# Performance work log

Measured on AMD Instinct MI355X. Metric: run time of the kernel, lower is better.

## Reference

```python
import jax, jax.numpy as jnp
import numpy as np

B, F, H, E, C, K = 32768, 1024, 512, 10, 10, 4  # batch, in_features, hidden, f_enc, num_classes, n_branches


def setup_inputs() -> dict:
    key = jax.random.key(0)
    ks = jax.random.split(key, 12)
    def rn(k, shape, scale):
        return jax.random.normal(k, shape, jnp.float32) * scale
    return {
        "w0": rn(ks[0], (B, F), 1.0),
        "w1": rn(ks[1], (B, F), 1.0),
        "w2": rn(ks[2], (B, F), 1.0),
        "w3": rn(ks[3], (B, F), 1.0),
        # 4 branch linears in -> hidden, stacked on leading axis
        "Wlin": rn(ks[4], (K, H, F), F ** -0.5),
        "blin": jnp.zeros((K, H), jnp.float32),
        # per-branch Q/K/V projections hidden -> f_enc
        "Wq": rn(ks[5], (K, E, H), H ** -0.5),
        "bq": jnp.zeros((K, E), jnp.float32),
        "Wk": rn(ks[6], (K, E, H), H ** -0.5),
        "bk": jnp.zeros((K, E), jnp.float32),
        "Wv": rn(ks[7], (K, E, H), H ** -0.5),
        "bv": jnp.zeros((K, E), jnp.float32),
        # 4 final classifier heads f_enc -> num_classes
        "Wfin": rn(ks[8], (K, C, E), E ** -0.5),
        "bfin": jnp.zeros((K, C), jnp.float32),
    }


def reference(w0, w1, w2, w3, Wlin, blin, Wq, bq, Wk, bk, Wv, bv, Wfin, bfin):
    # dropout is identity in eval mode
    w = jnp.stack([w0, w1, w2, w3], axis=1)              # [B,K,F]
    h = jnp.einsum('bkf,khf->bkh', w, Wlin) + blin        # [B,K,H]
    q = jnp.einsum('bkh,keh->bke', h, Wq) + bq            # [B,K,E]
    k_enc = jnp.einsum('bkh,keh->bke', h, Wk) + bk        # [B,K,E]
    v = jnp.einsum('bkh,keh->bke', h, Wv) + bv            # [B,K,E]
    # einsum 'bij,bil->bjl' contracts the branch axis (i == K)
    attn = jnp.einsum('bke,bkl->bel', q, k_enc) / np.float32(np.sqrt(E))  # [B,E,E]
    attn = jax.nn.softmax(attn, axis=1)                   # torch Softmax(dim=1)
    att_out = jnp.einsum('bnm,bkm->bkn', attn, v)         # [B,K,E]
    w0o = att_out[:, 0, :]                                # original uses index 0 for all four heads
    logits = jnp.einsum('be,kce->bkc', w0o, Wfin) + bfin  # [B,K,C]
    outputs = jnp.mean(jax.nn.softmax(logits, axis=-1), axis=1)  # 0.25 * sum of 4 softmaxed heads
    return (outputs, attn)
```

## Files before the change

kernel.cpp:

```cpp
#include <hip/hip_runtime.h>
#include <stdint.h>

#define B_ROWS 32768
#define F_DIM  1024
#define H_DIM  512
#define RS     32832

typedef __attribute__((ext_vector_type(4))) float    floatx4;
typedef __attribute__((ext_vector_type(2))) __fp16   fp16x2;
typedef __attribute__((ext_vector_type(8))) _Float16 halfx8;

__device__ __forceinline__ void async_load16(const void* g, void* l) {
    __builtin_amdgcn_global_load_lds(
        (const __attribute__((address_space(1))) void*)g,
        (__attribute__((address_space(3))) void*)l, 16, 0, 0);
}

__global__ __launch_bounds__(64) void k_prep(
    const float* __restrict__ Wlin, const float* __restrict__ blin,
    const float* __restrict__ Wq, const float* __restrict__ Wk,
    const float* __restrict__ Wv, const float* __restrict__ bq,
    const float* __restrict__ bk, const float* __restrict__ bv,
    ushort* __restrict__ Wcomb16, float* __restrict__ bcomb)
{
    __shared__ float sw_[H_DIM];
    __shared__ float sbl[H_DIM];
    const int bx = blockIdx.x;
    const int k  = bx >> 7;
    const int d  = (bx >> 2) & 31;
    const int qd = bx & 3;
    const int t  = threadIdx.x;
    const int col = qd * 256 + t * 4;
    ushort4* outp = (ushort4*)(Wcomb16 + (((size_t)(k * 32 + d)) << 10) + col);

    if (d >= 30) {
        ushort4 z; z.x = z.y = z.z = z.w = 0;
        *outp = z;
        if (qd == 0 && t == 0) bcomb[k * 32 + d] = 0.f;
        return;
    }

    const float* wrow; float bias;
    if (d < 10)      { wrow = Wq + (size_t)(k * 10 + d) * H_DIM;      bias = bq[k * 10 + d]; }
    else if (d < 20) { wrow = Wk + (size_t)(k * 10 + d - 10) * H_DIM; bias = bk[k * 10 + d - 10]; }
    else             { wrow = Wv + (size_t)(k * 10 + d - 20) * H_DIM; bias = bv[k * 10 + d - 20]; }

    const float* bl = blin + (size_t)k * H_DIM;
    for (int i = t; i < H_DIM; i += 64) { sw_[i] = wrow[i]; sbl[i] = bl[i]; }
    __syncthreads();

    const float* wl = Wlin + (((size_t)k * H_DIM) << 10) + col;

    floatx4 acc0 = {0.f,0.f,0.f,0.f}, acc1 = {0.f,0.f,0.f,0.f};
    float ba0 = 0.f, ba1 = 0.f;
    #pragma unroll 8
    for (int h = 0; h < H_DIM; h += 2) {
        const float s0 = sw_[h], s1 = sw_[h + 1];
        const floatx4 x0 = *(const floatx4*)(wl + ((size_t)h << 10));
        const floatx4 x1 = *(const floatx4*)(wl + ((size_t)(h + 1) << 10));
        acc0 += x0 * s0;
        acc1 += x1 * s1;
        ba0 += s0 * sbl[h];
        ba1 += s1 * sbl[h + 1];
    }
    const floatx4 acc = acc0 + acc1;
    union { _Float16 h[4]; ushort4 u; } o;
    o.h[0] = (_Float16)acc.x; o.h[1] = (_Float16)acc.y;
    o.h[2] = (_Float16)acc.z; o.h[3] = (_Float16)acc.w;
    *outp = o.u;
    if (qd == 0 && t == 0) bcomb[k * 32 + d] = bias + ba0 + ba1;
}

__global__ __launch_bounds__(512, 4) void k_main(
    const float* __restrict__ w0, const float* __restrict__ w1,
    const float* __restrict__ w2, const float* __restrict__ w3,
    const ushort* __restrict__ Wcomb16, const float* __restrict__ bcomb,
    float* __restrict__ qkv_t)
{
    __shared__ ushort Bs[32 * 1024];

    const int tid     = threadIdx.x;
    const int bx      = blockIdx.x;
    const int k       = bx & 3;
    const int rowBase = (bx >> 2) * 256;

    const float* A = (k == 0) ? w0 : (k == 1) ? w1 : (k == 2) ? w2 : w3;

    #pragma unroll
    for (int it = 0; it < 8; ++it) {
        const int s   = it * 512 + tid;
        const int row = s >> 7;
        const int g   = (s & 127) ^ (row & 7);
        async_load16(Wcomb16 + (((size_t)(k * 32 + row)) << 10) + g * 8,
                     (ushort*)Bs + (size_t)s * 8);
    }
    __syncthreads();

    const int wv = tid >> 6;
    const int ln = tid & 63;
    const int lr = ln & 15;
    const int lq = ln >> 4;
    const int sw = lr & 7;

    const float* aP0 = A + (size_t)(rowBase + wv * 32 + lr) * F_DIM + lq * 8;
    const float* aP1 = aP0 + (size_t)16 * F_DIM;

    floatx4 acc[2][2] = {};

#define LOADC(kc, b0, b1, b2, b3) do {                       \
    b0 = *(const floatx4*)(aP0 + (kc));                      \
    b1 = *(const floatx4*)(aP0 + (kc) + 4);                  \
    b2 = *(const floatx4*)(aP1 + (kc));                      \
    b3 = *(const floatx4*)(aP1 + (kc) + 4);                  \
} while (0)

#define COMPUTE(t, b0, b1, b2, b3) do {                                      \
    union { fp16x2 h2[4]; halfx8 h8; } u0, u1;                               \
    u0.h2[0] = __builtin_amdgcn_cvt_pkrtz(b0.x, b0.y);                       \
    u0.h2[1] = __builtin_amdgcn_cvt_pkrtz(b0.z, b0.w);                       \
    u0.h2[2] = __builtin_amdgcn_cvt_pkrtz(b1.x, b1.y);                       \
    u0.h2[3] = __builtin_amdgcn_cvt_pkrtz(b1.z, b1.w);                       \
    u1.h2[0] = __builtin_amdgcn_cvt_pkrtz(b2.x, b2.y);                       \
    u1.h2[1] = __builtin_amdgcn_cvt_pkrtz(b2.z, b2.w);                       \
    u1.h2[2] = __builtin_amdgcn_cvt_pkrtz(b3.x, b3.y);                       \
    u1.h2[3] = __builtin_amdgcn_cvt_pkrtz(b3.z, b3.w);                       \
    const int slot_ = (((t) * 4 + lq) ^ sw) * 8;                             \
    const halfx8 bf0 = *(const halfx8*)&Bs[(lr << 10) + slot_];              \
    const halfx8 bf1 = *(const halfx8*)&Bs[((16 + lr) << 10) + slot_];       \
    acc[0][0] = __builtin_amdgcn_mfma_f32_16x16x32_f16(u0.h8, bf0, acc[0][0], 0, 0, 0); \
    acc[0][1] = __builtin_amdgcn_mfma_f32_16x16x32_f16(u0.h8, bf1, acc[0][1], 0, 0, 0); \
    acc[1][0] = __builtin_amdgcn_mfma_f32_16x16x32_f16(u1.h8, bf0, acc[1][0], 0, 0, 0); \
    acc[1][1] = __builtin_amdgcn_mfma_f32_16x16x32_f16(u1.h8, bf1, acc[1][1], 0, 0, 0); \
} while (0)

    floatx4 a0, a1, a2, a3, c0, c1, c2, c3;
    LOADC(0, a0, a1, a2, a3);
    #pragma unroll 2
    for (int t = 0; t < 32; t += 2) {
        LOADC((t + 1) * 32, c0, c1, c2, c3);
        COMPUTE(t, a0, a1, a2, a3);
        if (t + 2 < 32) LOADC((t + 2) * 32, a0, a1, a2, a3);
        COMPUTE(t + 1, c0, c1, c2, c3);
    }
#undef LOADC
#undef COMPUTE

    const float* bc   = bcomb + k * 32;
    const int    dmax = (k == 0) ? 30 : 20;
    #pragma unroll
    for (int j = 0; j < 2; ++j) {
        const int d = j * 16 + lr;
        if (d < dmax) {
            const float bias = bc[d];
            float* outd = qkv_t + (size_t)(k * 30 + d) * RS;
            #pragma unroll
            for (int i = 0; i < 2; ++i) {
                const int r0 = rowBase + wv * 32 + i * 16 + lq * 4;
                floatx4 o = acc[i][j];
                o.x += bias; o.y += bias; o.z += bias; o.w += bias;
                *(floatx4*)(outd + r0) = o;
            }
        }
    }
}

__global__ __launch_bounds__(128) void k_final(
    const float* __restrict__ qkv_t, const float* __restrict__ Wfin,
    const float* __restrict__ bfin,
    float* __restrict__ outputs, float* __restrict__ attn)
{
    __shared__ float sW[400];
    __shared__ float sb[40];
    __shared__ float sA[128 * 101];
    const int t = threadIdx.x;
    for (int i = t; i < 400; i += 128) sW[i] = Wfin[i];
    if (t < 40) sb[t] = bfin[t];
    __syncthreads();

    const int b = blockIdx.x * 128 + t;
    const float* pt = qkv_t + b;
    float q[4][10], kk[4][10], v0[10];
    #pragma unroll
    for (int k = 0; k < 4; ++k)
        #pragma unroll
        for (int e = 0; e < 10; ++e) {
            q[k][e]  = pt[(size_t)(k * 30 + e) * RS];
            kk[k][e] = pt[(size_t)(k * 30 + 10 + e) * RS];
        }
    #pragma unroll
    for (int m = 0; m < 10; ++m) v0[m] = pt[(size_t)(20 + m) * RS];

    float out0[10];
    #pragma unroll
    for (int e = 0; e < 10; ++e) out0[e] = 0.f;
    float* sAr = &sA[t * 101];
    const float inv = 0.31622776601683794f;

    #pragma unroll
    for (int m = 0; m < 10; ++m) {
        float col[10]; float mx = -1e30f;
        #pragma unroll
        for (int e = 0; e < 10; ++e) {
            col[e] = (q[0][e]*kk[0][m] + q[1][e]*kk[1][m]
                    + q[2][e]*kk[2][m] + q[3][e]*kk[3][m]) * inv;
            mx = fmaxf(mx, col[e]);
        }
        float s = 0.f;
        #pragma unroll
        for (int e = 0; e < 10; ++e) { col[e] = __expf(col[e] - mx); s += col[e]; }
        const float r = 1.f / s;
        #pragma unroll
        for (int e = 0; e < 10; ++e) {
            const float a = col[e] * r;
            sAr[e * 10 + m] = a;
            out0[e] += a * v0[m];
        }
    }

    float oc[10];
    #pragma unroll
    for (int c = 0; c < 10; ++c) oc[c] = 0.f;
    #pragma unroll
    for (int k = 0; k < 4; ++k) {
        float lg[10]; float mx = -1e30f;
        #pragma unroll
        for (int c = 0; c < 10; ++c) {
            float s = sb[k * 10 + c];
            #pragma unroll
            for (int e = 0; e < 10; ++e) s += out0[e] * sW[(k * 10 + c) * 10 + e];
            lg[c] = s; mx = fmaxf(mx, s);
        }
        float s = 0.f;
        #pragma unroll
        for (int c = 0; c < 10; ++c) { lg[c] = __expf(lg[c] - mx); s += lg[c]; }
        const float r = 0.25f / s;
        #pragma unroll
        for (int c = 0; c < 10; ++c) oc[c] += lg[c] * r;
    }

    __syncthreads();
    const size_t abase = (size_t)blockIdx.x * 12800;
    for (int i = t; i < 12800; i += 128) {
        const int bl = i / 100;
        attn[abase + i] = sA[bl * 101 + (i - bl * 100)];
    }

    __syncthreads();
    #pragma unroll
    for (int c = 0; c < 10; ++c) sA[t * 11 + c] = oc[c];
    __syncthreads();
    const size_t obase = (size_t)blockIdx.x * 1280;
    for (int i = t; i < 1280; i += 128) {
        const int bl = i / 10;
        outputs[obase + i] = sA[bl * 11 + (i - bl * 10)];
    }
}

extern "C" void kernel_launch(void* const* d_in, const int* in_sizes, int n_in,
                              void* d_out, int out_size, void* d_ws, size_t ws_size,
                              hipStream_t stream) {
    const float* w0   = (const float*)d_in[0];
    const float* w1   = (const float*)d_in[1];
    const float* w2   = (const float*)d_in[2];
    const float* w3   = (const float*)d_in[3];
    const float* Wlin = (const float*)d_in[4];
    const float* blin = (const float*)d_in[5];
    const float* Wq   = (const float*)d_in[6];
    const float* bq   = (const float*)d_in[7];
    const float* Wk   = (const float*)d_in[8];
    const float* bk   = (const float*)d_in[9];
    const float* Wv   = (const float*)d_in[10];
    const float* bv   = (const float*)d_in[11];
    const float* Wfin = (const float*)d_in[12];
    const float* bfin = (const float*)d_in[13];

    char* ws = (char*)d_ws;
    ushort* Wcomb16 = (ushort*)ws;
    float*  bcomb   = (float*)(ws + ((size_t)256 << 10));
    float*  qkv_t   = (float*)(ws + ((size_t)1 << 20));

    float* outputs = (float*)d_out;
    float* attn    = outputs + (size_t)B_ROWS * 10;

    k_prep <<<512, 64,  0, stream>>>(Wlin, blin, Wq, Wk, Wv, bq, bk, bv, Wcomb16, bcomb);
    k_main <<<512, 512, 0, stream>>>(w0, w1, w2, w3, Wcomb16, bcomb, qkv_t);
    k_final<<<256, 128, 0, stream>>>(qkv_t, Wfin, bfin, outputs, attn);
}
```

Measured before the change: 583.1 us.

## Fuse projection GEMM with attention epilogue, keeping QKV in shared memory

Merges the main fp16 MFMA projection kernel and the attention/classifier kernel into one kernel. Each 512-thread block handles 128 rows and loops over the four branches, keeping the QKV activations in LDS instead of writing and rereading a transposed global buffer. The prep kernel also moves to 128-thread blocks covering half a row each. The grid shrinks to 256 blocks with about 130KB of LDS each, which lowers occupancy and latency hiding on the memory-bound input stream. Only a quarter of the threads do the attention epilogue, so that phase serialises after the GEMM.

After: 566.9 us. 1.03x faster.

```diff
diff --git a/kernel.cpp b/kernel.cpp
--- a/kernel.cpp
+++ b/kernel.cpp
@@ -4,7 +4,6 @@
 #define B_ROWS 32768
 #define F_DIM  1024
 #define H_DIM  512
-#define RS     32832
 
 typedef __attribute__((ext_vector_type(4))) float    floatx4;
 typedef __attribute__((ext_vector_type(2))) __fp16   fp16x2;
@@ -16,7 +15,7 @@
         (__attribute__((address_space(3))) void*)l, 16, 0, 0);
 }
 
-__global__ __launch_bounds__(64) void k_prep(
+__global__ __launch_bounds__(128) void k_prep(
     const float* __restrict__ Wlin, const float* __restrict__ blin,
     const float* __restrict__ Wq, const float* __restrict__ Wk,
     const float* __restrict__ Wv, const float* __restrict__ bq,
@@ -25,18 +24,18 @@
 {
     __shared__ float sw_[H_DIM];
     __shared__ float sbl[H_DIM];
-    const int bx = blockIdx.x;
-    const int k  = bx >> 7;
-    const int d  = (bx >> 2) & 31;
-    const int qd = bx & 3;
-    const int t  = threadIdx.x;
-    const int col = qd * 256 + t * 4;
+    const int bx   = blockIdx.x;
+    const int k    = bx >> 6;
+    const int d    = (bx >> 1) & 31;
+    const int half = bx & 1;
+    const int t    = threadIdx.x;
+    const int col  = half * 512 + t * 4;
     ushort4* outp = (ushort4*)(Wcomb16 + (((size_t)(k * 32 + d)) << 10) + col);
 
     if (d >= 30) {
         ushort4 z; z.x = z.y = z.z = z.w = 0;
         *outp = z;
-        if (qd == 0 && t == 0) bcomb[k * 32 + d] = 0.f;
+        if (half == 0 && t == 0) bcomb[k * 32 + d] = 0.f;
         return;
     }
 
@@ -46,7 +45,7 @@
     else             { wrow = Wv + (size_t)(k * 10 + d - 20) * H_DIM; bias = bv[k * 10 + d - 20]; }
 
     const float* bl = blin + (size_t)k * H_DIM;
-    for (int i = t; i < H_DIM; i += 64) { sw_[i] = wrow[i]; sbl[i] = bl[i]; }
+    for (int i = t; i < H_DIM; i += 128) { sw_[i] = wrow[i]; sbl[i] = bl[i]; }
     __syncthreads();
 
     const float* wl = Wlin + (((size_t)k * H_DIM) << 10) + col;
@@ -68,33 +67,37 @@
     o.h[0] = (_Float16)acc.x; o.h[1] = (_Float16)acc.y;
     o.h[2] = (_Float16)acc.z; o.h[3] = (_Float16)acc.w;
     *outp = o.u;
-    if (qd == 0 && t == 0) bcomb[k * 32 + d] = bias + ba0 + ba1;
-}
-
-__global__ __launch_bounds__(512, 4) void k_main(
+    if (half == 0 && t == 0) bcomb[k * 32 + d] = bias + ba0 + ba1;
+}
+
+#define SM_BS    0
+#define SM_QKV   (64 * 1024)
+#define SM_BC    (SM_QKV + 128 * 121 * 4)
+#define SM_W     (SM_BC + 512)
+#define SM_B     (SM_W + 1600)
+#define SM_TOTAL (SM_B + 160)
+
+__global__ __launch_bounds__(512) void k_all(
     const float* __restrict__ w0, const float* __restrict__ w1,
     const float* __restrict__ w2, const float* __restrict__ w3,
     const ushort* __restrict__ Wcomb16, const float* __restrict__ bcomb,
-    float* __restrict__ qkv_t)
+    const float* __restrict__ Wfin, const float* __restrict__ bfin,
+    float* __restrict__ outputs, float* __restrict__ attn)
 {
-    __shared__ ushort Bs[32 * 1024];
+    __shared__ __align__(16) unsigned char smem[SM_TOTAL];
+    ushort* Bs  = (ushort*)(smem + SM_BS);
+    float*  QKV = (float*) (smem + SM_QKV);
+    float*  sbc = (float*) (smem + SM_BC);
+    float*  sW  = (float*) (smem + SM_W);
+    float*  sb  = (float*) (smem + SM_B);
+    float*  sA  = (float*) (smem + SM_BS);
 
     const int tid     = threadIdx.x;
-    const int bx      = blockIdx.x;
-    const int k       = bx & 3;
-    const int rowBase = (bx >> 2) * 256;
-
-    const float* A = (k == 0) ? w0 : (k == 1) ? w1 : (k == 2) ? w2 : w3;
-
-    #pragma unroll
-    for (int it = 0; it < 8; ++it) {
-        const int s   = it * 512 + tid;
-        const int row = s >> 7;
-        const int g   = (s & 127) ^ (row & 7);
-        async_load16(Wcomb16 + (((size_t)(k * 32 + row)) << 10) + g * 8,
-                     (ushort*)Bs + (size_t)s * 8);
-    }
-    __syncthreads();
+    const int rowBase = blockIdx.x * 128;
+
+    if (tid < 128) sbc[tid] = bcomb[tid];
+    if (tid < 400) sW[tid]  = Wfin[tid];
+    if (tid < 40)  sb[tid]  = bfin[tid];
 
     const int wv = tid >> 6;
     const int ln = tid & 63;
@@ -102,155 +105,145 @@
     const int lq = ln >> 4;
     const int sw = lr & 7;
 
-    const float* aP0 = A + (size_t)(rowBase + wv * 32 + lr) * F_DIM + lq * 8;
-    const float* aP1 = aP0 + (size_t)16 * F_DIM;
-
-    floatx4 acc[2][2] = {};
-
-#define LOADC(kc, b0, b1, b2, b3) do {                       \
-    b0 = *(const floatx4*)(aP0 + (kc));                      \
-    b1 = *(const floatx4*)(aP0 + (kc) + 4);                  \
-    b2 = *(const floatx4*)(aP1 + (kc));                      \
-    b3 = *(const floatx4*)(aP1 + (kc) + 4);                  \
-} while (0)
-
-#define COMPUTE(t, b0, b1, b2, b3) do {                                      \
-    union { fp16x2 h2[4]; halfx8 h8; } u0, u1;                               \
-    u0.h2[0] = __builtin_amdgcn_cvt_pkrtz(b0.x, b0.y);                       \
-    u0.h2[1] = __builtin_amdgcn_cvt_pkrtz(b0.z, b0.w);                       \
-    u0.h2[2] = __builtin_amdgcn_cvt_pkrtz(b1.x, b1.y);                       \
-    u0.h2[3] = __builtin_amdgcn_cvt_pkrtz(b1.z, b1.w);                       \
-    u1.h2[0] = __builtin_amdgcn_cvt_pkrtz(b2.x, b2.y);                       \
-    u1.h2[1] = __builtin_amdgcn_cvt_pkrtz(b2.z, b2.w);                       \
-    u1.h2[2] = __builtin_amdgcn_cvt_pkrtz(b3.x, b3.y);                       \
-    u1.h2[3] = __builtin_amdgcn_cvt_pkrtz(b3.z, b3.w);                       \
+    #pragma unroll 1
+    for (int k = 0; k < 4; ++k) {
+        const float* A = (k == 0) ? w0 : (k == 1) ? w1 : (k == 2) ? w2 : w3;
+
+        __syncthreads();
+        #pragma unroll
+        for (int it = 0; it < 8; ++it) {
+            const int s   = it * 512 + tid;
+            const int row = s >> 7;
+            const int g   = (s & 127) ^ (row & 7);
+            async_load16(Wcomb16 + (((size_t)(k * 32 + row)) << 10) + g * 8,
+                         (ushort*)Bs + (size_t)s * 8);
+        }
+        __syncthreads();
+
+        const float* aP = A + (size_t)(rowBase + wv * 16 + lr) * F_DIM + lq * 8;
+
+        floatx4 acc0 = {0.f,0.f,0.f,0.f};
+        floatx4 acc1 = {0.f,0.f,0.f,0.f};
+
+#define COMPUTE(t, b0, b1) do {                                              \
+    union { fp16x2 h2[4]; halfx8 h8; } u;                                    \
+    u.h2[0] = __builtin_amdgcn_cvt_pkrtz(b0.x, b0.y);                        \
+    u.h2[1] = __builtin_amdgcn_cvt_pkrtz(b0.z, b0.w);                        \
+    u.h2[2] = __builtin_amdgcn_cvt_pkrtz(b1.x, b1.y);                        \
+    u.h2[3] = __builtin_amdgcn_cvt_pkrtz(b1.z, b1.w);                        \
     const int slot_ = (((t) * 4 + lq) ^ sw) * 8;                             \
     const halfx8 bf0 = *(const halfx8*)&Bs[(lr << 10) + slot_];              \
     const halfx8 bf1 = *(const halfx8*)&Bs[((16 + lr) << 10) + slot_];       \
-    acc[0][0] = __builtin_amdgcn_mfma_f32_16x16x32_f16(u0.h8, bf0, acc[0][0], 0, 0, 0); \
-    acc[0][1] = __builtin_amdgcn_mfma_f32_16x16x32_f16(u0.h8, bf1, acc[0][1], 0, 0, 0); \
-    acc[1][0] = __builtin_amdgcn_mfma_f32_16x16x32_f16(u1.h8, bf0, acc[1][0], 0, 0, 0); \
-    acc[1][1] = __builtin_amdgcn_mfma_f32_16x16x32_f16(u1.h8, bf1, acc[1][1], 0, 0, 0); \
+    acc0 = __builtin_amdgcn_mfma_f32_16x16x32_f16(u.h8, bf0, acc0, 0, 0, 0); \
+    acc1 = __builtin_amdgcn_mfma_f32_16x16x32_f16(u.h8, bf1, acc1, 0, 0, 0); \
 } while (0)
 
-    floatx4 a0, a1, a2, a3, c0, c1, c2, c3;
-    LOADC(0, a0, a1, a2, a3);
-    #pragma unroll 2
-    for (int t = 0; t < 32; t += 2) {
-        LOADC((t + 1) * 32, c0, c1, c2, c3);
-        COMPUTE(t, a0, a1, a2, a3);
-        if (t + 2 < 32) LOADC((t + 2) * 32, a0, a1, a2, a3);
-        COMPUTE(t + 1, c0, c1, c2, c3);
-    }
-#undef LOADC
+        floatx4 a0, a1, c0, c1;
+        a0 = *(const floatx4*)(aP);
+        a1 = *(const floatx4*)(aP + 4);
+        #pragma unroll 4
+        for (int t = 0; t < 32; t += 2) {
+            c0 = *(const floatx4*)(aP + (t + 1) * 32);
+            c1 = *(const floatx4*)(aP + (t + 1) * 32 + 4);
+            COMPUTE(t, a0, a1);
+            if (t + 2 < 32) {
+                a0 = *(const floatx4*)(aP + (t + 2) * 32);
+                a1 = *(const floatx4*)(aP + (t + 2) * 32 + 4);
+            }
+            COMPUTE(t + 1, c0, c1);
+        }
 #undef COMPUTE
 
-    const float* bc   = bcomb + k * 32;
-    const int    dmax = (k == 0) ? 30 : 20;
-    #pragma unroll
-    for (int j = 0; j < 2; ++j) {
-        const int d = j * 16 + lr;
-        if (d < dmax) {
-            const float bias = bc[d];
-            float* outd = qkv_t + (size_t)(k * 30 + d) * RS;
-            #pragma unroll
-            for (int i = 0; i < 2; ++i) {
-                const int r0 = rowBase + wv * 32 + i * 16 + lq * 4;
-                floatx4 o = acc[i][j];
-                o.x += bias; o.y += bias; o.z += bias; o.w += bias;
-                *(floatx4*)(outd + r0) = o;
-            }
-        }
-    }
-}
-
-__global__ __launch_bounds__(128) void k_final(
-    const float* __restrict__ qkv_t, const float* __restrict__ Wfin,
-    const float* __restrict__ bfin,
-    float* __restrict__ outputs, float* __restrict__ attn)
-{
-    __shared__ float sW[400];
-    __shared__ float sb[40];
-    __shared__ float sA[128 * 101];
-    const int t = threadIdx.x;
-    for (int i = t; i < 400; i += 128) sW[i] = Wfin[i];
-    if (t < 40) sb[t] = bfin[t];
-    __syncthreads();
-
-    const int b = blockIdx.x * 128 + t;
-    const float* pt = qkv_t + b;
-    float q[4][10], kk[4][10], v0[10];
-    #pragma unroll
-    for (int k = 0; k < 4; ++k)
-        #pragma unroll
-        for (int e = 0; e < 10; ++e) {
-            q[k][e]  = pt[(size_t)(k * 30 + e) * RS];
-            kk[k][e] = pt[(size_t)(k * 30 + 10 + e) * RS];
-        }
-    #pragma unroll
-    for (int m = 0; m < 10; ++m) v0[m] = pt[(size_t)(20 + m) * RS];
-
-    float out0[10];
-    #pragma unroll
-    for (int e = 0; e < 10; ++e) out0[e] = 0.f;
-    float* sAr = &sA[t * 101];
-    const float inv = 0.31622776601683794f;
-
-    #pragma unroll
-    for (int m = 0; m < 10; ++m) {
-        float col[10]; float mx = -1e30f;
-        #pragma unroll
-        for (int e = 0; e < 10; ++e) {
-            col[e] = (q[0][e]*kk[0][m] + q[1][e]*kk[1][m]
-                    + q[2][e]*kk[2][m] + q[3][e]*kk[3][m]) * inv;
-            mx = fmaxf(mx, col[e]);
-        }
-        float s = 0.f;
-        #pragma unroll
-        for (int e = 0; e < 10; ++e) { col[e] = __expf(col[e] - mx); s += col[e]; }
-        const float r = 1.f / s;
-        #pragma unroll
-        for (int e = 0; e < 10; ++e) {
-            const float a = col[e] * r;
-            sAr[e * 10 + m] = a;
-            out0[e] += a * v0[m];
-        }
-    }
+        const int r0 = wv * 16 + lq * 4;
+        #pragma unroll
+        for (int r = 0; r < 4; ++r)
+            QKV[(r0 + r) * 121 + k * 30 + lr] = acc0[r] + sbc[k * 32 + lr];
+        const int d1 = 16 + lr;
+        if (d1 < ((k == 0) ? 30 : 20)) {
+            #pragma unroll
+            for (int r = 0; r < 4; ++r)
+                QKV[(r0 + r) * 121 + k * 30 + d1] = acc1[r] + sbc[k * 32 + d1];
+        }
+    }
+    __syncthreads();
 
     float oc[10];
-    #pragma unroll
-    for (int c = 0; c < 10; ++c) oc[c] = 0.f;
-    #pragma unroll
-    for (int k = 0; k < 4; ++k) {
-        float lg[10]; float mx = -1e30f;
-        #pragma unroll
-        for (int c = 0; c < 10; ++c) {
-            float s = sb[k * 10 + c];
-            #pragma unroll
-            for (int e = 0; e < 10; ++e) s += out0[e] * sW[(k * 10 + c) * 10 + e];
-            lg[c] = s; mx = fmaxf(mx, s);
-        }
-        float s = 0.f;
-        #pragma unroll
-        for (int c = 0; c < 10; ++c) { lg[c] = __expf(lg[c] - mx); s += lg[c]; }
-        const float r = 0.25f / s;
-        #pragma unroll
-        for (int c = 0; c < 10; ++c) oc[c] += lg[c] * r;
+    if (tid < 128) {
+        const float* Q = &QKV[tid * 121];
+        float q[4][10], kk[4][10], v0[10];
+        #pragma unroll
+        for (int k = 0; k < 4; ++k)
+            #pragma unroll
+            for (int e = 0; e < 10; ++e) {
+                q[k][e]  = Q[k * 30 + e];
+                kk[k][e] = Q[k * 30 + 10 + e];
+            }
+        #pragma unroll
+        for (int m = 0; m < 10; ++m) v0[m] = Q[20 + m];
+
+        float out0[10];
+        #pragma unroll
+        for (int e = 0; e < 10; ++e) out0[e] = 0.f;
+        float* sAr = &sA[tid * 101];
+        const float inv = 0.31622776601683794f;
+
+        #pragma unroll
+        for (int m = 0; m < 10; ++m) {
+            float col[10]; float mx = -1e30f;
+            #pragma unroll
+            for (int e = 0; e < 10; ++e) {
+                col[e] = (q[0][e]*kk[0][m] + q[1][e]*kk[1][m]
+                        + q[2][e]*kk[2][m] + q[3][e]*kk[3][m]) * inv;
+                mx = fmaxf(mx, col[e]);
+            }
+            float s = 0.f;
+            #pragma unroll
+            for (int e = 0; e < 10; ++e) { col[e] = __expf(col[e] - mx); s += col[e]; }
+            const float r = 1.f / s;
+            #pragma unroll
+            for (int e = 0; e < 10; ++e) {
+                const float a = col[e] * r;
+                sAr[e * 10 + m] = a;
+                out0[e] += a * v0[m];
+            }
+        }
+
+        #pragma unroll
+        for (int c = 0; c < 10; ++c) oc[c] = 0.f;
+        #pragma unroll
+        for (int k = 0; k < 4; ++k) {
+            float lg[10]; float mx = -1e30f;
+            #pragma unroll
+            for (int c = 0; c < 10; ++c) {
+                float s = sb[k * 10 + c];
+                #pragma unroll
+                for (int e = 0; e < 10; ++e) s += out0[e] * sW[(k * 10 + c) * 10 + e];
+                lg[c] = s; mx = fmaxf(mx, s);
+            }
+            float s = 0.f;
+            #pragma unroll
+            for (int c = 0; c < 10; ++c) { lg[c] = __expf(lg[c] - mx); s += lg[c]; }
+            const float r = 0.25f / s;
+            #pragma unroll
+            for (int c = 0; c < 10; ++c) oc[c] += lg[c] * r;
+        }
     }
 
     __syncthreads();
     const size_t abase = (size_t)blockIdx.x * 12800;
-    for (int i = t; i < 12800; i += 128) {
+    for (int i = tid; i < 12800; i += 512) {
         const int bl = i / 100;
         attn[abase + i] = sA[bl * 101 + (i - bl * 100)];
     }
 
     __syncthreads();
-    #pragma unroll
-    for (int c = 0; c < 10; ++c) sA[t * 11 + c] = oc[c];
+    if (tid < 128) {
+        #pragma unroll
+        for (int c = 0; c < 10; ++c) sA[tid * 11 + c] = oc[c];
+    }
     __syncthreads();
     const size_t obase = (size_t)blockIdx.x * 1280;
-    for (int i = t; i < 1280; i += 128) {
+    for (int i = tid; i < 1280; i += 512) {
         const int bl = i / 10;
         outputs[obase + i] = sA[bl * 11 + (i - bl * 10)];
     }
@@ -277,12 +270,10 @@
     char* ws = (char*)d_ws;
     ushort* Wcomb16 = (ushort*)ws;
     float*  bcomb   = (float*)(ws + ((size_t)256 << 10));
-    float*  qkv_t   = (float*)(ws + ((size_t)1 << 20));
 
     float* outputs = (float*)d_out;
     float* attn    = outputs + (size_t)B_ROWS * 10;
 
-    k_prep <<<512, 64,  0, stream>>>(Wlin, blin, Wq, Wk, Wv, bq, bk, bv, Wcomb16, bcomb);
-    k_main <<<512, 512, 0, stream>>>(w0, w1, w2, w3, Wcomb16, bcomb, qkv_t);
-    k_final<<<256, 128, 0, stream>>>(qkv_t, Wfin, bfin, outputs, attn);
-}
+    k_prep<<<256, 128, 0, stream>>>(Wlin, blin, Wq, Wk, Wv, bq, bk, bv, Wcomb16, bcomb);
+    k_all <<<256, 512, 0, stream>>>(w0, w1, w2, w3, Wcomb16, bcomb, Wfin, bfin, outputs, attn);
+}
```
